# Performance work log

Hardware: AMD Instinct MI355X
Metric: run time of the kernel (lower is better)

Reference implementation:

```python
import jax, jax.numpy as jnp
import numpy as np

N_HEAD = 16


def setup_inputs() -> dict:
    key = jax.random.key(0)
    k1, k2, k3 = jax.random.split(key, 3)
    B, T, C = 4, 2048, 1024
    x = jax.random.normal(k1, (B, T, C), dtype=jnp.float32)
    Wqkv = jax.random.normal(k2, (C, 3 * C), dtype=jnp.float32) * 0.02
    Wproj = jax.random.normal(k3, (C, C), dtype=jnp.float32) * 0.02
    return {"x": x, "Wqkv": Wqkv, "Wproj": Wproj}


def reference(x, Wqkv, Wproj):
    B, T, C = x.shape
    nh = N_HEAD
    hd = C // nh
    qkv = x @ Wqkv                                  # (B, T, 3C)
    q, k, v = jnp.split(qkv, 3, axis=-1)
    # (B, T, C) -> (B, nh, T, hd)
    q = q.reshape(B, T, nh, hd).transpose(0, 2, 1, 3)
    k = k.reshape(B, T, nh, hd).transpose(0, 2, 1, 3)
    v = v.reshape(B, T, nh, hd).transpose(0, 2, 1, 3)
    # scaled dot-product attention with causal mask (past_kv=None => T_all == T)
    att = jnp.einsum("bhtd,bhsd->bhts", q, k) / jnp.sqrt(jnp.float32(hd))
    causal = jnp.tril(jnp.ones((T, T), dtype=bool))  # (T, T)
    att = jnp.where(causal[None, None, :, :], att, jnp.float32(-jnp.inf))
    att = jax.nn.softmax(att, axis=-1)              # (B, nh, T, T)
    y = jnp.einsum("bhts,bhsd->bhtd", att, v)       # (B, nh, T, hd)
    y = y.transpose(0, 2, 1, 3).reshape(B, T, C)
    y = y @ Wproj                                   # (B, T, C)
    # present_kv (detached in original)
    return y, jax.lax.stop_gradient(k), jax.lax.stop_gradient(v)
```

## Files before the change

kernel.cpp:

```cpp
#include <hip/hip_runtime.h>
#include <hip/hip_bf16.h>


typedef __bf16 bf16;
typedef __attribute__((ext_vector_type(8))) __bf16 bf16x8;
typedef __attribute__((ext_vector_type(4))) __bf16 bf16x4;
typedef __attribute__((ext_vector_type(4))) float f32x4;

#define AS_G __attribute__((address_space(1)))
#define AS_L __attribute__((address_space(3)))

#define QSCALE 0.1803368801111204f

__device__ __forceinline__ void gld_lds16(const bf16* g, bf16* l) {
  __builtin_amdgcn_global_load_lds((const AS_G void*)g, (AS_L void*)l, 16, 0, 0);
}

__global__ __launch_bounds__(256) void k_cast(const float* __restrict__ in,
                                              bf16* __restrict__ out, int n) {
  int i = (blockIdx.x * 256 + threadIdx.x) * 8;
  if (i >= n) return;
  float4 a = *(const float4*)(in + i);
  float4 b = *(const float4*)(in + i + 4);
  bf16x8 o;
  o[0] = (bf16)a.x; o[1] = (bf16)a.y; o[2] = (bf16)a.z; o[3] = (bf16)a.w;
  o[4] = (bf16)b.x; o[5] = (bf16)b.y; o[6] = (bf16)b.z; o[7] = (bf16)b.w;
  *(bf16x8*)(out + i) = o;
}

__global__ __launch_bounds__(256) void k_transpose(const float* __restrict__ in,
                                                   bf16* __restrict__ out,
                                                   int K, int N) {
  __shared__ float tile[32][33];
  int bx = blockIdx.x * 32;
  int by = blockIdx.y * 32;
  int tx = threadIdx.x, ty = threadIdx.y;
#pragma unroll
  for (int i = 0; i < 4; ++i)
    tile[ty + i * 8][tx] = in[(size_t)(by + ty + i * 8) * N + bx + tx];
  __syncthreads();
#pragma unroll
  for (int i = 0; i < 4; ++i)
    out[(size_t)(bx + ty + i * 8) * K + by + tx] = (bf16)tile[tx][ty + i * 8];
}

__device__ __forceinline__ void gemm_tile_128(const bf16* __restrict__ A,
                                              const bf16* __restrict__ Bt,
                                              int m0, int n0,
                                              bf16* As, bf16* Bs,
                                              f32x4 acc[4][4]) {
  const int tid = threadIdx.x;
  const int w = tid >> 6, lane = tid & 63, lo = lane & 15, hi = lane >> 4;
  const int wm = w >> 1, wn = w & 1;
#pragma unroll 1
  for (int k0 = 0; k0 < 1024; k0 += 32) {
#pragma unroll
    for (int p = 0; p < 2; ++p) {
      int u = tid + 256 * p;
      int row = u >> 2, cs = u & 3;
      int g = cs ^ ((row >> 1) & 3);
      gld_lds16(A + (size_t)(m0 + row) * 1024 + k0 + g * 8, As + p * 2048 + w * 512);
      gld_lds16(Bt + (size_t)(n0 + row) * 1024 + k0 + g * 8, Bs + p * 2048 + w * 512);
    }
    __syncthreads();
    bf16x8 af[4], bfr[4];
#pragma unroll
    for (int i = 0; i < 4; ++i) {
      int row = wm * 64 + i * 16 + lo;
      af[i] = *(const bf16x8*)(As + row * 32 + (hi ^ ((row >> 1) & 3)) * 8);
    }
#pragma unroll
    for (int j = 0; j < 4; ++j) {
      int row = wn * 64 + j * 16 + lo;
      bfr[j] = *(const bf16x8*)(Bs + row * 32 + (hi ^ ((row >> 1) & 3)) * 8);
    }
#pragma unroll
    for (int i = 0; i < 4; ++i)
#pragma unroll
      for (int j = 0; j < 4; ++j)
        acc[i][j] = __builtin_amdgcn_mfma_f32_16x16x32_bf16(af[i], bfr[j], acc[i][j], 0, 0, 0);
    __syncthreads();
  }
}

__global__ __launch_bounds__(256) void k_gemm_qkv(const bf16* __restrict__ x,
                                                  const bf16* __restrict__ WqkvT,
                                                  bf16* __restrict__ qb, bf16* __restrict__ kb,
                                                  bf16* __restrict__ vtb,
                                                  float* __restrict__ outk, float* __restrict__ outv) {
  __shared__ bf16 As[128 * 32], Bs[128 * 32];
  f32x4 acc[4][4] = {};
  int m0 = blockIdx.y * 128, n0 = blockIdx.x * 128;
  gemm_tile_128(x, WqkvT, m0, n0, As, Bs, acc);
  const int tid = threadIdx.x;
  const int w = tid >> 6, lane = tid & 63, lo = lane & 15, hi = lane >> 4;
  const int wm = w >> 1, wn = w & 1;
#pragma unroll
  for (int i = 0; i < 4; ++i) {
    int growbase = m0 + wm * 64 + i * 16 + hi * 4;
    int b = growbase >> 11, t0 = growbase & 2047;
#pragma unroll
    for (int j = 0; j < 4; ++j) {
      int gcol = n0 + wn * 64 + j * 16 + lo;
      int part = gcol >> 10;
      int cc = gcol & 1023, h = cc >> 6, d = cc & 63;
      size_t idx0 = ((size_t)(b * 16 + h) * 2048 + t0) * 64 + d;
      if (part == 0) {
#pragma unroll
        for (int r = 0; r < 4; ++r) qb[idx0 + (size_t)r * 64] = (bf16)(acc[i][j][r] * QSCALE);
      } else if (part == 1) {
#pragma unroll
        for (int r = 0; r < 4; ++r) {
          float val = acc[i][j][r];
          kb[idx0 + (size_t)r * 64] = (bf16)val;
          outk[idx0 + (size_t)r * 64] = val;
        }
      } else {
        bf16x4 pk;
#pragma unroll
        for (int r = 0; r < 4; ++r) {
          float val = acc[i][j][r];
          outv[idx0 + (size_t)r * 64] = val;
          pk[r] = (bf16)val;
        }
        *(bf16x4*)(vtb + ((size_t)(b * 16 + h) * 64 + d) * 2048 + t0) = pk;
      }
    }
  }
}

__global__ __launch_bounds__(256) void k_gemm_proj(const bf16* __restrict__ yb,
                                                   const bf16* __restrict__ WprojT,
                                                   float* __restrict__ out) {
  __shared__ bf16 As[128 * 32], Bs[128 * 32];
  f32x4 acc[4][4] = {};
  int m0 = blockIdx.y * 128, n0 = blockIdx.x * 128;
  gemm_tile_128(yb, WprojT, m0, n0, As, Bs, acc);
  const int tid = threadIdx.x;
  const int w = tid >> 6, lane = tid & 63, lo = lane & 15, hi = lane >> 4;
  const int wm = w >> 1, wn = w & 1;
#pragma unroll
  for (int i = 0; i < 4; ++i)
#pragma unroll
    for (int j = 0; j < 4; ++j)
#pragma unroll
      for (int r = 0; r < 4; ++r) {
        int grow = m0 + wm * 64 + i * 16 + hi * 4 + r;
        int gcol = n0 + wn * 64 + j * 16 + lo;
        out[(size_t)grow * 1024 + gcol] = acc[i][j][r];
      }
}

__device__ __forceinline__ void p_store(f32x4 sacc[4], bool mask,
                                        int w, int lo, int hi, bf16* psrow) {
  if (mask) {
#pragma unroll
    for (int nt = 0; nt < 4; ++nt)
#pragma unroll
      for (int r = 0; r < 4; ++r)
        if (nt * 16 + hi * 4 + r > w * 16 + lo) sacc[nt][r] = -1e30f;
  }
#pragma unroll
  for (int nt = 0; nt < 4; ++nt) {
    bf16x4 pk;
#pragma unroll
    for (int r = 0; r < 4; ++r) pk[r] = (bf16)exp2f(sacc[nt][r]);
    *(bf16x4*)(psrow + (w * 16 + lo) * 72 + nt * 16 + hi * 4) = pk;
  }
}

__device__ __forceinline__ void write_y(bf16* __restrict__ y, int b, int h, int qrow,
                                        int hi, const f32x4 o[4], float inv) {
  size_t base = ((size_t)b * 2048 + qrow) * 1024 + h * 64;
#pragma unroll
  for (int mt = 0; mt < 4; ++mt) {
    bf16x4 yk;
#pragma unroll
    for (int r = 0; r < 4; ++r) yk[r] = (bf16)(o[mt][r] * inv);
    *(bf16x4*)(y + base + mt * 16 + hi * 4) = yk;
  }
}

__global__ __launch_bounds__(256, 4) void k_flash(const bf16* __restrict__ q,
                                                  const bf16* __restrict__ k,
                                                  const bf16* __restrict__ vt,
                                                  bf16* __restrict__ y) {
  __shared__ bf16 Ks[64 * 64];
  __shared__ bf16 Vs[80 * 64];
  __shared__ bf16 Ps[128 * 72];
  const int bi = blockIdx.x;
  const int slot = bi >> 3;
  const int bh = (bi & 7) + 8 * (slot >> 4);
  const int j = slot & 15;
  const int jA = j, jB = 31 - j;
  const int tid = threadIdx.x, w = tid >> 6, lane = tid & 63, lo = lane & 15, hi = lane >> 4;
  const bf16* qp = q + (size_t)bh * 2048 * 64;
  const bf16* kp = k + (size_t)bh * 2048 * 64;
  const bf16* vtp = vt + (size_t)bh * 64 * 2048;

  {
    int rr = tid >> 4, c = (tid & 15) * 4;
    bf16x4 z;
    bf16 v1 = (rr == 0) ? (bf16)1.0f : (bf16)0.0f;
    z[0] = v1; z[1] = v1; z[2] = v1; z[3] = v1;
    *(bf16x4*)(Vs + (64 + rr) * 64 + c) = z;
  }

  bf16x8 qfA[2], qfB[2];
  {
    int qA = jA * 64 + w * 16 + lo;
    int qB = jB * 64 + w * 16 + lo;
    qfA[0] = *(const bf16x8*)(qp + (size_t)qA * 64 + hi * 8);
    qfA[1] = *(const bf16x8*)(qp + (size_t)qA * 64 + 32 + hi * 8);
    qfB[0] = *(const bf16x8*)(qp + (size_t)qB * 64 + hi * 8);
    qfB[1] = *(const bf16x8*)(qp + (size_t)qB * 64 + 32 + hi * 8);
  }
  f32x4 oA[4] = {}, oB[4] = {};
  f32x4 oLA = {}, oLB = {};

  for (int st = 0; st <= jB; ++st) {
    const int s0 = st * 64;
#pragma unroll
    for (int p = 0; p < 2; ++p) {
      int u = tid + 256 * p;
      int row = u >> 3, c = u & 7, g = c ^ (row & 7);
      gld_lds16(kp + (size_t)(s0 + row) * 64 + g * 8, Ks + p * 2048 + w * 512);
      gld_lds16(vtp + (size_t)row * 2048 + s0 + g * 8, Vs + p * 2048 + w * 512);
    }
    __syncthreads();

    bf16x8 kf[4][2];
#pragma unroll
    for (int nt = 0; nt < 4; ++nt)
#pragma unroll
      for (int ks = 0; ks < 2; ++ks)
        kf[nt][ks] = *(const bf16x8*)(Ks + (nt * 16 + lo) * 64 + ((ks * 4 + hi) ^ (lo & 7)) * 8);

    const bool actA = (st <= jA);
    if (actA) {
      f32x4 sacc[4] = {};
#pragma unroll
      for (int nt = 0; nt < 4; ++nt)
#pragma unroll
        for (int ks = 0; ks < 2; ++ks)
          sacc[nt] = __builtin_amdgcn_mfma_f32_16x16x32_bf16(kf[nt][ks], qfA[ks], sacc[nt], 0, 0, 0);
      p_store(sacc, st == jA, w, lo, hi, Ps);
    }
    {
      f32x4 sacc[4] = {};
#pragma unroll
      for (int nt = 0; nt < 4; ++nt)
#pragma unroll
        for (int ks = 0; ks < 2; ++ks)
          sacc[nt] = __builtin_amdgcn_mfma_f32_16x16x32_bf16(kf[nt][ks], qfB[ks], sacc[nt], 0, 0, 0);
      p_store(sacc, st == jB, w, lo, hi, Ps + 64 * 72);
    }
    __asm__ volatile("s_waitcnt lgkmcnt(0)" ::: "memory");

    bf16x8 pfA[2], pfB[2];
#pragma unroll
    for (int ks = 0; ks < 2; ++ks) {
      pfB[ks] = *(const bf16x8*)(Ps + (64 + w * 16 + lo) * 72 + ks * 32 + hi * 8);
      if (actA) pfA[ks] = *(const bf16x8*)(Ps + (w * 16 + lo) * 72 + ks * 32 + hi * 8);
    }
#pragma unroll
    for (int mt = 0; mt < 5; ++mt) {
#pragma unroll
      for (int ks = 0; ks < 2; ++ks) {
        int row = mt * 16 + lo;
        bf16x8 vf = *(const bf16x8*)(Vs + row * 64 + ((ks * 4 + hi) ^ (row & 7)) * 8);
        if (mt < 4) {
          oB[mt] = __builtin_amdgcn_mfma_f32_16x16x32_bf16(vf, pfB[ks], oB[mt], 0, 0, 0);
          if (actA) oA[mt] = __builtin_amdgcn_mfma_f32_16x16x32_bf16(vf, pfA[ks], oA[mt], 0, 0, 0);
        } else {
          oLB = __builtin_amdgcn_mfma_f32_16x16x32_bf16(vf, pfB[ks], oLB, 0, 0, 0);
          if (actA) oLA = __builtin_amdgcn_mfma_f32_16x16x32_bf16(vf, pfA[ks], oLA, 0, 0, 0);
        }
      }
    }
    __syncthreads();
  }

  const int b = bh >> 4, h = bh & 15;
  float lA = __shfl(oLA[0], lo, 64);
  float lB = __shfl(oLB[0], lo, 64);
  write_y(y, b, h, jA * 64 + w * 16 + lo, hi, oA, 1.0f / lA);
  write_y(y, b, h, jB * 64 + w * 16 + lo, hi, oB, 1.0f / lB);
}

extern "C" void kernel_launch(void* const* d_in, const int* in_sizes, int n_in,
                              void* d_out, int out_size, void* d_ws, size_t ws_size,
                              hipStream_t stream) {
  const float* x = (const float*)d_in[0];
  const float* Wqkv = (const float*)d_in[1];
  const float* Wproj = (const float*)d_in[2];
  float* out = (float*)d_out;

  const size_t YSZ = (size_t)8192 * 1024;
  char* ws = (char*)d_ws;
  bf16* xb = (bf16*)ws;      ws += (size_t)8192 * 1024 * 2;
  bf16* wqkvT = (bf16*)ws;   ws += (size_t)3072 * 1024 * 2;
  bf16* wprojT = (bf16*)ws;  ws += (size_t)1024 * 1024 * 2;
  bf16* qb = (bf16*)ws;      ws += (size_t)64 * 2048 * 64 * 2;
  bf16* kb = (bf16*)ws;      ws += (size_t)64 * 2048 * 64 * 2;
  bf16* vtb = (bf16*)ws;     ws += (size_t)64 * 2048 * 64 * 2;
  bf16* yb = (bf16*)ws;

  float* outy = out;
  float* outk = out + YSZ;
  float* outv = out + 2 * YSZ;

  k_cast<<<4096, 256, 0, stream>>>(x, xb, 8388608);
  dim3 tb(32, 8);
  k_transpose<<<dim3(96, 32), tb, 0, stream>>>(Wqkv, wqkvT, 1024, 3072);
  k_transpose<<<dim3(32, 32), tb, 0, stream>>>(Wproj, wprojT, 1024, 1024);
  k_gemm_qkv<<<dim3(24, 64), 256, 0, stream>>>(xb, wqkvT, qb, kb, vtb, outk, outv);
  k_flash<<<1024, 256, 0, stream>>>(qb, kb, vtb, yb);
  k_gemm_proj<<<dim3(8, 64), 256, 0, stream>>>(yb, wprojT, outy);
}
```

Measured before the change: 323.1 us.

## Rewrite flash attention with 32x32 MFMA, register P, double-buffered KV

Merges the cast and two transposes into one prep kernel, and folds the Q scale into the transposed Wqkv weights instead of the GEMM epilogue. The flash kernel moves to 32x32x16 MFMA with four query tiles per block and keeps P in registers, exchanging halves via cross-lane shuffles instead of going through LDS. It also double-buffers the K/V LDS staging so loads overlap compute, and computes the row sum directly rather than through an extra ones-row MFMA. The aim is fewer launches, less LDS traffic and fewer barriers, at the cost of higher register pressure (occupancy hint lowered to 2) and half as many blocks.

```diff
diff --git a/kernel.cpp b/kernel.cpp
--- a/kernel.cpp
+++ b/kernel.cpp
@@ -6,6 +6,7 @@
 typedef __attribute__((ext_vector_type(8))) __bf16 bf16x8;
 typedef __attribute__((ext_vector_type(4))) __bf16 bf16x4;
 typedef __attribute__((ext_vector_type(4))) float f32x4;
+typedef __attribute__((ext_vector_type(16))) float f32x16;
 
 #define AS_G __attribute__((address_space(1)))
 #define AS_L __attribute__((address_space(3)))
@@ -16,32 +17,38 @@
   __builtin_amdgcn_global_load_lds((const AS_G void*)g, (AS_L void*)l, 16, 0, 0);
 }
 
-__global__ __launch_bounds__(256) void k_cast(const float* __restrict__ in,
-                                              bf16* __restrict__ out, int n) {
-  int i = (blockIdx.x * 256 + threadIdx.x) * 8;
-  if (i >= n) return;
-  float4 a = *(const float4*)(in + i);
-  float4 b = *(const float4*)(in + i + 4);
-  bf16x8 o;
-  o[0] = (bf16)a.x; o[1] = (bf16)a.y; o[2] = (bf16)a.z; o[3] = (bf16)a.w;
-  o[4] = (bf16)b.x; o[5] = (bf16)b.y; o[6] = (bf16)b.z; o[7] = (bf16)b.w;
-  *(bf16x8*)(out + i) = o;
-}
-
-__global__ __launch_bounds__(256) void k_transpose(const float* __restrict__ in,
-                                                   bf16* __restrict__ out,
-                                                   int K, int N) {
+__global__ __launch_bounds__(256) void k_prep(const float* __restrict__ x,
+                                              const float* __restrict__ Wqkv,
+                                              const float* __restrict__ Wproj,
+                                              bf16* __restrict__ xb,
+                                              bf16* __restrict__ wqkvT,
+                                              bf16* __restrict__ wprojT) {
+  const int bid = blockIdx.x, tid = threadIdx.x;
+  if (bid < 4096) {
+    int i = (bid * 256 + tid) * 8;
+    float4 a = *(const float4*)(x + i);
+    float4 b = *(const float4*)(x + i + 4);
+    bf16x8 o;
+    o[0] = (bf16)a.x; o[1] = (bf16)a.y; o[2] = (bf16)a.z; o[3] = (bf16)a.w;
+    o[4] = (bf16)b.x; o[5] = (bf16)b.y; o[6] = (bf16)b.z; o[7] = (bf16)b.w;
+    *(bf16x8*)(xb + i) = o;
+    return;
+  }
   __shared__ float tile[32][33];
-  int bx = blockIdx.x * 32;
-  int by = blockIdx.y * 32;
-  int tx = threadIdx.x, ty = threadIdx.y;
+  const float* in; bf16* outp; int N, bx, by; bool isqkv;
+  if (bid < 7168) { int t = bid - 4096; in = Wqkv; outp = wqkvT; N = 3072; bx = (t % 96) * 32; by = (t / 96) * 32; isqkv = true; }
+  else            { int t = bid - 7168; in = Wproj; outp = wprojT; N = 1024; bx = (t % 32) * 32; by = (t / 32) * 32; isqkv = false; }
+  const int tx = tid & 31, ty = tid >> 5;
 #pragma unroll
   for (int i = 0; i < 4; ++i)
     tile[ty + i * 8][tx] = in[(size_t)(by + ty + i * 8) * N + bx + tx];
   __syncthreads();
 #pragma unroll
-  for (int i = 0; i < 4; ++i)
-    out[(size_t)(bx + ty + i * 8) * K + by + tx] = (bf16)tile[tx][ty + i * 8];
+  for (int i = 0; i < 4; ++i) {
+    int n = bx + ty + i * 8;
+    float s = (isqkv && n < 1024) ? QSCALE : 1.0f;
+    outp[(size_t)n * 1024 + by + tx] = (bf16)(tile[tx][ty + i * 8] * s);
+  }
 }
 
 __device__ __forceinline__ void gemm_tile_128(const bf16* __restrict__ A,
@@ -107,7 +114,7 @@
       size_t idx0 = ((size_t)(b * 16 + h) * 2048 + t0) * 64 + d;
       if (part == 0) {
 #pragma unroll
-        for (int r = 0; r < 4; ++r) qb[idx0 + (size_t)r * 64] = (bf16)(acc[i][j][r] * QSCALE);
+        for (int r = 0; r < 4; ++r) qb[idx0 + (size_t)r * 64] = (bf16)acc[i][j][r];
       } else if (part == 1) {
 #pragma unroll
         for (int r = 0; r < 4; ++r) {
@@ -151,141 +158,148 @@
       }
 }
 
-__device__ __forceinline__ void p_store(f32x4 sacc[4], bool mask,
-                                        int w, int lo, int hi, bf16* psrow) {
-  if (mask) {
-#pragma unroll
-    for (int nt = 0; nt < 4; ++nt)
-#pragma unroll
-      for (int r = 0; r < 4; ++r)
-        if (nt * 16 + hi * 4 + r > w * 16 + lo) sacc[nt][r] = -1e30f;
-  }
-#pragma unroll
-  for (int nt = 0; nt < 4; ++nt) {
+__device__ __forceinline__ void stage_kv(const bf16* kp, const bf16* vtp,
+                                         bf16* KsD, bf16* VsD, int st, int tid, int w) {
+  const int s0 = st * 64;
+#pragma unroll
+  for (int pp = 0; pp < 2; ++pp) {
+    int u = tid + 256 * pp;
+    int row = u >> 3, c = u & 7, g = c ^ (row & 7);
+    gld_lds16(kp + (size_t)(s0 + row) * 64 + g * 8, KsD + pp * 2048 + w * 512);
+    gld_lds16(vtp + (size_t)row * 2048 + s0 + g * 8, VsD + pp * 2048 + w * 512);
+  }
+}
+
+__device__ __forceinline__ void soft_pack(const f32x16& sa, bool mk, int sbase, int qg,
+                                          int hi, float& l, uint2 uo[4], uint2 ux[4]) {
+#pragma unroll
+  for (int g = 0; g < 4; ++g) {
     bf16x4 pk;
 #pragma unroll
-    for (int r = 0; r < 4; ++r) pk[r] = (bf16)exp2f(sacc[nt][r]);
-    *(bf16x4*)(psrow + (w * 16 + lo) * 72 + nt * 16 + hi * 4) = pk;
-  }
-}
-
-__device__ __forceinline__ void write_y(bf16* __restrict__ y, int b, int h, int qrow,
-                                        int hi, const f32x4 o[4], float inv) {
-  size_t base = ((size_t)b * 2048 + qrow) * 1024 + h * 64;
-#pragma unroll
-  for (int mt = 0; mt < 4; ++mt) {
+    for (int c = 0; c < 4; ++c) {
+      float ev = exp2f(sa[4 * g + c]);
+      if (mk) { int sg = sbase + c + 8 * g + 4 * hi; if (sg > qg) ev = 0.f; }
+      bf16 pb = (bf16)ev;
+      pk[c] = pb;
+      l += (float)pb;
+    }
+    uint2 uu; __builtin_memcpy(&uu, &pk, 8);
+    uo[g] = uu;
+    ux[g].x = __shfl_xor(uu.x, 32, 64);
+    ux[g].y = __shfl_xor(uu.y, 32, 64);
+  }
+}
+
+__device__ __forceinline__ bf16x8 asm_b(int hi, uint2 own, uint2 rcv) {
+  unsigned int r[4];
+  if (hi == 0) { r[0] = own.x; r[1] = own.y; r[2] = rcv.x; r[3] = rcv.y; }
+  else         { r[0] = rcv.x; r[1] = rcv.y; r[2] = own.x; r[3] = own.y; }
+  bf16x8 b; __builtin_memcpy(&b, r, 16); return b;
+}
+
+__device__ __forceinline__ void wr_o(bf16* __restrict__ y, size_t base, int dbase, int hi,
+                                     const f32x16& O, float inv) {
+#pragma unroll
+  for (int g = 0; g < 4; ++g) {
     bf16x4 yk;
 #pragma unroll
-    for (int r = 0; r < 4; ++r) yk[r] = (bf16)(o[mt][r] * inv);
-    *(bf16x4*)(y + base + mt * 16 + hi * 4) = yk;
-  }
-}
-
-__global__ __launch_bounds__(256, 4) void k_flash(const bf16* __restrict__ q,
+    for (int c = 0; c < 4; ++c) yk[c] = (bf16)(O[4 * g + c] * inv);
+    *(bf16x4*)(y + base + dbase + 8 * g + 4 * hi) = yk;
+  }
+}
+
+__global__ __launch_bounds__(256, 2) void k_flash(const bf16* __restrict__ q,
                                                   const bf16* __restrict__ k,
                                                   const bf16* __restrict__ vt,
                                                   bf16* __restrict__ y) {
-  __shared__ bf16 Ks[64 * 64];
-  __shared__ bf16 Vs[80 * 64];
-  __shared__ bf16 Ps[128 * 72];
+  __shared__ bf16 Ks[2][64 * 64];
+  __shared__ bf16 Vs[2][64 * 64];
   const int bi = blockIdx.x;
-  const int slot = bi >> 3;
-  const int bh = (bi & 7) + 8 * (slot >> 4);
-  const int j = slot & 15;
-  const int jA = j, jB = 31 - j;
-  const int tid = threadIdx.x, w = tid >> 6, lane = tid & 63, lo = lane & 15, hi = lane >> 4;
+  const int bh = (bi & 7) + 8 * (bi >> 6);
+  const int m = (bi >> 3) & 7;
+  const int j1 = 2 * m, j2 = 2 * m + 1, jB2 = 30 - 2 * m, jB1 = 31 - 2 * m;
+  const int tid = threadIdx.x, w = tid >> 6, lane = tid & 63;
+  const int col = lane & 31, hi = lane >> 5, sub = col & 15, half = col >> 4;
   const bf16* qp = q + (size_t)bh * 2048 * 64;
   const bf16* kp = k + (size_t)bh * 2048 * 64;
   const bf16* vtp = vt + (size_t)bh * 64 * 2048;
 
-  {
-    int rr = tid >> 4, c = (tid & 15) * 4;
-    bf16x4 z;
-    bf16 v1 = (rr == 0) ? (bf16)1.0f : (bf16)0.0f;
-    z[0] = v1; z[1] = v1; z[2] = v1; z[3] = v1;
-    *(bf16x4*)(Vs + (64 + rr) * 64 + c) = z;
-  }
-
-  bf16x8 qfA[2], qfB[2];
-  {
-    int qA = jA * 64 + w * 16 + lo;
-    int qB = jB * 64 + w * 16 + lo;
-    qfA[0] = *(const bf16x8*)(qp + (size_t)qA * 64 + hi * 8);
-    qfA[1] = *(const bf16x8*)(qp + (size_t)qA * 64 + 32 + hi * 8);
-    qfB[0] = *(const bf16x8*)(qp + (size_t)qB * 64 + hi * 8);
-    qfB[1] = *(const bf16x8*)(qp + (size_t)qB * 64 + 32 + hi * 8);
-  }
-  f32x4 oA[4] = {}, oB[4] = {};
-  f32x4 oLA = {}, oLB = {};
-
-  for (int st = 0; st <= jB; ++st) {
+  const int qg0 = (half ? jB1 : jB2) * 64 + w * 16 + sub;
+  const int qg1 = (half ? j2 : j1) * 64 + w * 16 + sub;
+
+  bf16x8 qf0[4], qf1[4];
+#pragma unroll
+  for (int kc = 0; kc < 4; ++kc) {
+    qf0[kc] = *(const bf16x8*)(qp + (size_t)qg0 * 64 + kc * 16 + hi * 8);
+    qf1[kc] = *(const bf16x8*)(qp + (size_t)qg1 * 64 + kc * 16 + hi * 8);
+  }
+
+  f32x16 O00 = {}, O10 = {}, O01 = {}, O11 = {};
+  float l0 = 0.f, l1 = 0.f;
+
+  stage_kv(kp, vtp, Ks[0], Vs[0], 0, tid, w);
+
+  for (int st = 0; st <= jB1; ++st) {
+    const int p = st & 1;
     const int s0 = st * 64;
-#pragma unroll
-    for (int p = 0; p < 2; ++p) {
-      int u = tid + 256 * p;
-      int row = u >> 3, c = u & 7, g = c ^ (row & 7);
-      gld_lds16(kp + (size_t)(s0 + row) * 64 + g * 8, Ks + p * 2048 + w * 512);
-      gld_lds16(vtp + (size_t)row * 2048 + s0 + g * 8, Vs + p * 2048 + w * 512);
-    }
     __syncthreads();
-
-    bf16x8 kf[4][2];
-#pragma unroll
-    for (int nt = 0; nt < 4; ++nt)
-#pragma unroll
-      for (int ks = 0; ks < 2; ++ks)
-        kf[nt][ks] = *(const bf16x8*)(Ks + (nt * 16 + lo) * 64 + ((ks * 4 + hi) ^ (lo & 7)) * 8);
-
-    const bool actA = (st <= jA);
-    if (actA) {
-      f32x4 sacc[4] = {};
-#pragma unroll
-      for (int nt = 0; nt < 4; ++nt)
-#pragma unroll
-        for (int ks = 0; ks < 2; ++ks)
-          sacc[nt] = __builtin_amdgcn_mfma_f32_16x16x32_bf16(kf[nt][ks], qfA[ks], sacc[nt], 0, 0, 0);
-      p_store(sacc, st == jA, w, lo, hi, Ps);
-    }
-    {
-      f32x4 sacc[4] = {};
-#pragma unroll
-      for (int nt = 0; nt < 4; ++nt)
-#pragma unroll
-        for (int ks = 0; ks < 2; ++ks)
-          sacc[nt] = __builtin_amdgcn_mfma_f32_16x16x32_bf16(kf[nt][ks], qfB[ks], sacc[nt], 0, 0, 0);
-      p_store(sacc, st == jB, w, lo, hi, Ps + 64 * 72);
-    }
-    __asm__ volatile("s_waitcnt lgkmcnt(0)" ::: "memory");
-
-    bf16x8 pfA[2], pfB[2];
-#pragma unroll
-    for (int ks = 0; ks < 2; ++ks) {
-      pfB[ks] = *(const bf16x8*)(Ps + (64 + w * 16 + lo) * 72 + ks * 32 + hi * 8);
-      if (actA) pfA[ks] = *(const bf16x8*)(Ps + (w * 16 + lo) * 72 + ks * 32 + hi * 8);
-    }
-#pragma unroll
-    for (int mt = 0; mt < 5; ++mt) {
-#pragma unroll
-      for (int ks = 0; ks < 2; ++ks) {
-        int row = mt * 16 + lo;
-        bf16x8 vf = *(const bf16x8*)(Vs + row * 64 + ((ks * 4 + hi) ^ (row & 7)) * 8);
-        if (mt < 4) {
-          oB[mt] = __builtin_amdgcn_mfma_f32_16x16x32_bf16(vf, pfB[ks], oB[mt], 0, 0, 0);
-          if (actA) oA[mt] = __builtin_amdgcn_mfma_f32_16x16x32_bf16(vf, pfA[ks], oA[mt], 0, 0, 0);
-        } else {
-          oLB = __builtin_amdgcn_mfma_f32_16x16x32_bf16(vf, pfB[ks], oLB, 0, 0, 0);
-          if (actA) oLA = __builtin_amdgcn_mfma_f32_16x16x32_bf16(vf, pfA[ks], oLA, 0, 0, 0);
+    if (st < jB1) stage_kv(kp, vtp, Ks[p ^ 1], Vs[p ^ 1], st + 1, tid, w);
+    const bool act1 = (st <= j2);
+    const bf16* KsP = Ks[p];
+    const bf16* VsP = Vs[p];
+#pragma unroll
+    for (int St = 0; St < 2; ++St) {
+      const int sbase = s0 + St * 32;
+      f32x16 sa0 = {}, sa1 = {};
+#pragma unroll
+      for (int kc = 0; kc < 4; ++kc) {
+        int srow = St * 32 + col;
+        int cc = kc * 2 + hi;
+        bf16x8 kfr = *(const bf16x8*)(KsP + srow * 64 + ((cc ^ (srow & 7)) * 8));
+        sa0 = __builtin_amdgcn_mfma_f32_32x32x16_bf16(kfr, qf0[kc], sa0, 0, 0, 0);
+        if (act1) sa1 = __builtin_amdgcn_mfma_f32_32x32x16_bf16(kfr, qf1[kc], sa1, 0, 0, 0);
+      }
+      const bool mk0 = (sbase + 31) > (jB2 * 64 + w * 16);
+      const bool mk1 = (sbase + 31) > (j1 * 64 + w * 16);
+      uint2 u0[4], x0[4], u1[4], x1[4];
+      soft_pack(sa0, mk0, sbase, qg0, hi, l0, u0, x0);
+      if (act1) soft_pack(sa1, mk1, sbase, qg1, hi, l1, u1, x1);
+#pragma unroll
+      for (int t = 0; t < 2; ++t) {
+        bf16x8 b0 = asm_b(hi, u0[2 * t + hi], x0[2 * t + hi]);
+        bf16x8 b1 = b0;
+        if (act1) b1 = asm_b(hi, u1[2 * t + hi], x1[2 * t + hi]);
+        int cc2 = (St * 2 + t) * 2 + hi;
+#pragma unroll
+        for (int Dt = 0; Dt < 2; ++Dt) {
+          int vrow = Dt * 32 + col;
+          bf16x8 vfr = *(const bf16x8*)(VsP + vrow * 64 + ((cc2 ^ (vrow & 7)) * 8));
+          if (Dt == 0) {
+            O00 = __builtin_amdgcn_mfma_f32_32x32x16_bf16(vfr, b0, O00, 0, 0, 0);
+            if (act1) O01 = __builtin_amdgcn_mfma_f32_32x32x16_bf16(vfr, b1, O01, 0, 0, 0);
+          } else {
+            O10 = __builtin_amdgcn_mfma_f32_32x32x16_bf16(vfr, b0, O10, 0, 0, 0);
+            if (act1) O11 = __builtin_amdgcn_mfma_f32_32x32x16_bf16(vfr, b1, O11, 0, 0, 0);
+          }
         }
       }
     }
-    __syncthreads();
-  }
-
+  }
+
+  const float lt0 = l0 + __shfl_xor(l0, 32, 64);
+  const float lt1 = l1 + __shfl_xor(l1, 32, 64);
+  const float inv0 = 1.0f / lt0, inv1 = 1.0f / lt1;
   const int b = bh >> 4, h = bh & 15;
-  float lA = __shfl(oLA[0], lo, 64);
-  float lB = __shfl(oLB[0], lo, 64);
-  write_y(y, b, h, jA * 64 + w * 16 + lo, hi, oA, 1.0f / lA);
-  write_y(y, b, h, jB * 64 + w * 16 + lo, hi, oB, 1.0f / lB);
+  {
+    size_t base = ((size_t)b * 2048 + qg0) * 1024 + h * 64;
+    wr_o(y, base, 0, hi, O00, inv0);
+    wr_o(y, base, 32, hi, O10, inv0);
+  }
+  {
+    size_t base = ((size_t)b * 2048 + qg1) * 1024 + h * 64;
+    wr_o(y, base, 0, hi, O01, inv1);
+    wr_o(y, base, 32, hi, O11, inv1);
+  }
 }
 
 extern "C" void kernel_launch(void* const* d_in, const int* in_sizes, int n_in,
@@ -310,11 +324,8 @@
   float* outk = out + YSZ;
   float* outv = out + 2 * YSZ;
 
-  k_cast<<<4096, 256, 0, stream>>>(x, xb, 8388608);
-  dim3 tb(32, 8);
-  k_transpose<<<dim3(96, 32), tb, 0, stream>>>(Wqkv, wqkvT, 1024, 3072);
-  k_transpose<<<dim3(32, 32), tb, 0, stream>>>(Wproj, wprojT, 1024, 1024);
+  k_prep<<<8192, 256, 0, stream>>>(x, Wqkv, Wproj, xb, wqkvT, wprojT);
   k_gemm_qkv<<<dim3(24, 64), 256, 0, stream>>>(xb, wqkvT, qb, kb, vtb, outk, outv);
-  k_flash<<<1024, 256, 0, stream>>>(qb, kb, vtb, yb);
+  k_flash<<<512, 256, 0, stream>>>(qb, kb, vtb, yb);
   k_gemm_proj<<<dim3(8, 64), 256, 0, stream>>>(yb, wprojT, outy);
 }
```

Result: slower. 402.3 us (+24.5%).
